# Kernel tuning notes

Hardware: AMD Instinct MI355X
Metric: run time of the kernel (lower is better)

## Reference

```python
import jax, jax.numpy as jnp
import numpy as np

IN_CH, OUT_CH, K = 4096, 4096, 64
C, F = IN_CH // K, OUT_CH // K  # 64, 64
BS = 256


def setup_inputs() -> dict:
    key = jax.random.key(0)
    k1, k2 = jax.random.split(key)
    x = jax.random.normal(k1, (BS, IN_CH), dtype=jnp.float32)
    stdv = 1.0 / float(np.sqrt(C))  # matches torch init: uniform(-1/sqrt(in_channels), ...)
    weights = jax.random.uniform(k2, (F, C, K), dtype=jnp.float32, minval=-stdv, maxval=stdv)
    return {"x": x, "weights": weights}


def reference(x, weights):
    # Faithful, batched version of Linear_BC_func.forward:
    #   per sample: ifft(fft(w, 'ortho') * fft(x, 'backward'), 'ortho').real, summed over C.
    # The per-sample Python loop and the C-sum are fused: sum over C is done in the
    # frequency domain (linearity of ifft), and the batch is handled by one einsum.
    bs = x.shape[0]
    f, c, k = weights.shape
    xk = x.reshape(bs, c, k)
    Wf = jnp.fft.fft(weights, norm="ortho")      # (F, C, K) complex64
    Xf = jnp.fft.fft(xk, norm="backward")        # (BS, C, K) complex64
    Sf = jnp.einsum("fck,bck->bfk", Wf, Xf)      # sum over C in frequency domain
    out = jnp.fft.ifft(Sf, norm="ortho").real.astype(jnp.float32)  # torch .float() keeps real part
    return out.reshape(bs, f * k)
```

## Files before the change

### kernel.cpp

```cpp
#include <hip/hip_runtime.h>


#define KDIM 4096

typedef __attribute__((ext_vector_type(8)))  short s16x8;
typedef __attribute__((ext_vector_type(4)))  float f32x4;
typedef __attribute__((ext_vector_type(16))) float f32x16;
typedef unsigned short u16;

__device__ __forceinline__ u16 f2bf(float f) {
  unsigned int u = __float_as_uint(f);
  u += 0x7FFF + ((u >> 16) & 1);
  return (u16)(u >> 16);
}

__global__ __launch_bounds__(256) void pack_kernel(const float* __restrict__ x,
                                                   u16* __restrict__ Xp) {
  __shared__ __align__(16) u16 tile[32 * 264];
  const int tid = threadIdx.x;
  const int rg  = blockIdx.x >> 4;
  const int cg  = blockIdx.x & 15;

  #pragma unroll
  for (int i = 0; i < 4; ++i) {
    int g    = i * 2048 + tid * 8;
    int row  = g >> 8;
    int kloc = g & 255;
    const float4* src = (const float4*)(x + (size_t)(rg * 32 + row) * 4096 + cg * 256 + kloc);
    float4 v0 = src[0], v1 = src[1];
    union { u16 u[8]; uint4 v; } o;
    o.u[0] = f2bf(v0.x); o.u[1] = f2bf(v0.y); o.u[2] = f2bf(v0.z); o.u[3] = f2bf(v0.w);
    o.u[4] = f2bf(v1.x); o.u[5] = f2bf(v1.y); o.u[6] = f2bf(v1.z); o.u[7] = f2bf(v1.w);
    *(uint4*)(tile + row * 264 + kloc) = o.v;
  }
  __syncthreads();

  const int lane = tid & 63;
  const int fw   = tid >> 6;
  #pragma unroll
  for (int i = 0; i < 4; ++i) {
    int fidx = i * 4 + fw;
    int cl   = fidx >> 2;
    int kk   = fidx & 3;
    int c    = cg * 4 + cl;
    uint4 v = *(const uint4*)(tile + (lane & 31) * 264 + cl * 64 + kk * 16 + (lane >> 5) * 8);
    size_t u = ((size_t)((c * 8 + rg) * 4 + kk) << 6) + lane;
    *(uint4*)(Xp + (u << 3)) = v;
  }
}

__global__ __launch_bounds__(1024, 4) void gemm_cnt(const u16* __restrict__ Xp,
                                                    const float* __restrict__ w,
                                                    float* __restrict__ out) {
  extern __shared__ __align__(16) char pool[];
  u16*   tab = (u16*)pool;
  float* red = (float*)pool;

  const int tid   = threadIdx.x;
  const int lane  = tid & 63;
  const int wid   = tid >> 6;
  const int cslot = wid & 7;
  const int half  = wid >> 3;
  const int l31   = lane & 31;
  const int lh    = lane >> 5;
  const int f     = blockIdx.x >> 2;
  const int q     = blockIdx.x & 3;
  const int rg    = q * 2 + half;

  const float* wf = w + ((size_t)f << 12);
  #pragma unroll
  for (int j = 0; j < 4; ++j) {
    int c = wid * 4 + j;
    u16 bv = f2bf(wf[(c << 6) + lane]);
    u16* T = tab + c * 576;
    #pragma unroll
    for (int m = 0; m < 8; ++m) {
      int i = (-(lane + m)) & 63;
      T[m * 72 + i] = bv;
    }
  }

  int bofs0, bofs1, bofs2, bofs3;
  {
    int i0;
    i0 = (lh * 8 - l31)      & 63; bofs0 = (i0 & 7) * 71 + i0;
    i0 = (lh * 8 - l31 - 16) & 63; bofs1 = (i0 & 7) * 71 + i0;
    i0 = (lh * 8 - l31 - 32) & 63; bofs2 = (i0 & 7) * 71 + i0;
    i0 = (lh * 8 - l31 - 48) & 63; bofs3 = (i0 & 7) * 71 + i0;
  }

  const u16* abase = Xp + ((size_t)(cslot * 8 + rg) * 2048 + lane * 8);

  s16x8 A0_0, A0_1, A0_2, A0_3;
  s16x8 A1_0, A1_1, A1_2, A1_3;
  s16x8 A2_0, A2_1, A2_2, A2_3;

  #define ALOAD(SET, T)                                                   \
    { const u16* nb_ = abase + (size_t)(T) * 131072;                      \
      asm volatile("global_load_dwordx4 %0, %4, off\n\t"                  \
                   "global_load_dwordx4 %1, %4, off offset:1024\n\t"      \
                   "global_load_dwordx4 %2, %4, off offset:2048\n\t"      \
                   "global_load_dwordx4 %3, %4, off offset:3072"          \
                   : "=&v"(A##SET##_0), "=&v"(A##SET##_1),                \
                     "=&v"(A##SET##_2), "=&v"(A##SET##_3)                 \
                   : "v"(nb_)); }

  #define WAITV_(N) asm volatile("s_waitcnt vmcnt(" #N ")")
  #define WAITV(N)  WAITV_(N)

  f32x16 acc0 = {}, acc1 = {};

  __syncthreads();

  ALOAD(0, 0)
  ALOAD(1, 1)

  #define STEP(T, CUR, PRE, DOPRE, WN)                                        \
    {                                                                         \
      if (DOPRE) ALOAD(PRE, (T) + 2)                                          \
      const u16* Tb = tab + (8 * (T) + cslot) * 576;                          \
      s16x8 b0 = *(const s16x8*)(Tb + bofs0);                                 \
      s16x8 b1 = *(const s16x8*)(Tb + bofs1);                                 \
      s16x8 b2 = *(const s16x8*)(Tb + bofs2);                                 \
      s16x8 b3 = *(const s16x8*)(Tb + bofs3);                                 \
      WAITV(WN);                                                              \
      __builtin_amdgcn_sched_barrier(0);                                      \
      acc0 = __builtin_amdgcn_mfma_f32_32x32x16_bf16(A##CUR##_0, b0, acc0, 0, 0, 0); \
      acc1 = __builtin_amdgcn_mfma_f32_32x32x16_bf16(A##CUR##_0, b2, acc1, 0, 0, 0); \
      acc0 = __builtin_amdgcn_mfma_f32_32x32x16_bf16(A##CUR##_1, b3, acc0, 0, 0, 0); \
      acc1 = __builtin_amdgcn_mfma_f32_32x32x16_bf16(A##CUR##_1, b1, acc1, 0, 0, 0); \
      acc0 = __builtin_amdgcn_mfma_f32_32x32x16_bf16(A##CUR##_2, b2, acc0, 0, 0, 0); \
      acc1 = __builtin_amdgcn_mfma_f32_32x32x16_bf16(A##CUR##_2, b0, acc1, 0, 0, 0); \
      acc0 = __builtin_amdgcn_mfma_f32_32x32x16_bf16(A##CUR##_3, b1, acc0, 0, 0, 0); \
      acc1 = __builtin_amdgcn_mfma_f32_32x32x16_bf16(A##CUR##_3, b3, acc1, 0, 0, 0); \
    }

  STEP(0, 0, 2, 1, 8)
  STEP(1, 1, 0, 1, 8)
  STEP(2, 2, 1, 1, 8)
  STEP(3, 0, 2, 1, 8)
  STEP(4, 1, 0, 1, 8)
  STEP(5, 2, 1, 1, 8)
  STEP(6, 0, 2, 0, 4)
  STEP(7, 1, 2, 0, 0)

  __syncthreads();
  {
    float* slot = red + wid * 2048;
    #pragma unroll
    for (int i = 0; i < 4; ++i) {
      f32x4 v0 = {acc0[4*i], acc0[4*i+1], acc0[4*i+2], acc0[4*i+3]};
      f32x4 v1 = {acc1[4*i], acc1[4*i+1], acc1[4*i+2], acc1[4*i+3]};
      *(f32x4*)(slot + ((i)     * 64 + lane) * 4) = v0;
      *(f32x4*)(slot + ((i + 4) * 64 + lane) * 4) = v1;
    }
  }
  __syncthreads();
  {
    const int rhalf = tid >> 9;
    const int ii    = (tid >> 6) & 7;
    const int sl    = tid & 63;
    f32x4 s = {};
    #pragma unroll
    for (int cs = 0; cs < 8; ++cs)
      s += *(const f32x4*)(red + (size_t)(rhalf * 8 + cs) * 2048 + (ii * 64 + sl) * 4);
    const int col  = (f << 6) + (ii >> 2) * 32 + (sl & 31);
    const int rowb = q * 64 + rhalf * 32 + 4 * (sl >> 5) + 8 * (ii & 3);
    #pragma unroll
    for (int e = 0; e < 4; ++e)
      out[(size_t)(rowb + e) * 4096 + col] = s[e];
  }
}

extern "C" void kernel_launch(void* const* d_in, const int* in_sizes, int n_in,
                              void* d_out, int out_size, void* d_ws, size_t ws_size,
                              hipStream_t stream) {
  const float* x = (const float*)d_in[0];
  const float* w = (const float*)d_in[1];
  float* out = (float*)d_out;

  u16* Xp = (u16*)d_ws;

  pack_kernel<<<128, 256, 0, stream>>>(x, Xp);
  gemm_cnt<<<256, 1024, 131072, stream>>>(Xp, w, out);
}
```

Baseline: 19.24 us.

## Retile circulant GEMM so each block covers two filters and 32 batch rows

```diff
diff --git a/kernel.cpp b/kernel.cpp
--- a/kernel.cpp
+++ b/kernel.cpp
@@ -49,9 +49,9 @@
   }
 }
 
-__global__ __launch_bounds__(1024, 4) void gemm_cnt(const u16* __restrict__ Xp,
-                                                    const float* __restrict__ w,
-                                                    float* __restrict__ out) {
+__global__ __launch_bounds__(1024, 4) void gemm_f2(const u16* __restrict__ Xp,
+                                                   const float* __restrict__ w,
+                                                   float* __restrict__ out) {
   extern __shared__ __align__(16) char pool[];
   u16*   tab = (u16*)pool;
   float* red = (float*)pool;
@@ -59,20 +59,20 @@
   const int tid   = threadIdx.x;
   const int lane  = tid & 63;
   const int wid   = tid >> 6;
-  const int cslot = wid & 7;
-  const int half  = wid >> 3;
+  const int cg    = wid & 1;
+  const int kg    = wid >> 1;
   const int l31   = lane & 31;
   const int lh    = lane >> 5;
-  const int f     = blockIdx.x >> 2;
-  const int q     = blockIdx.x & 3;
-  const int rg    = q * 2 + half;
+  const int q     = blockIdx.x & 7;
+  const int fg    = blockIdx.x >> 3;
 
-  const float* wf = w + ((size_t)f << 12);
   #pragma unroll
-  for (int j = 0; j < 4; ++j) {
-    int c = wid * 4 + j;
-    u16 bv = f2bf(wf[(c << 6) + lane]);
-    u16* T = tab + c * 576;
+  for (int j = 0; j < 8; ++j) {
+    int t    = wid * 8 + j;
+    int fidx = t >> 6;
+    int c    = t & 63;
+    u16 bv = f2bf(w[((size_t)(fg * 2 + fidx) << 12) + (c << 6) + lane]);
+    u16* T = tab + t * 576;
     #pragma unroll
     for (int m = 0; m < 8; ++m) {
       int i = (-(lane + m)) & 63;
@@ -89,14 +89,15 @@
     i0 = (lh * 8 - l31 - 48) & 63; bofs3 = (i0 & 7) * 71 + i0;
   }
 
-  const u16* abase = Xp + ((size_t)(cslot * 8 + rg) * 2048 + lane * 8);
+  const u16* abase = Xp + ((size_t)kg * 8 * 16384 + q * 2048 + lane * 8);
+  const u16* tabf  = tab + cg * 36864;
 
   s16x8 A0_0, A0_1, A0_2, A0_3;
   s16x8 A1_0, A1_1, A1_2, A1_3;
   s16x8 A2_0, A2_1, A2_2, A2_3;
 
   #define ALOAD(SET, T)                                                   \
-    { const u16* nb_ = abase + (size_t)(T) * 131072;                      \
+    { const u16* nb_ = abase + (size_t)(T) * 16384;                       \
       asm volatile("global_load_dwordx4 %0, %4, off\n\t"                  \
                    "global_load_dwordx4 %1, %4, off offset:1024\n\t"      \
                    "global_load_dwordx4 %2, %4, off offset:2048\n\t"      \
@@ -118,7 +119,7 @@
   #define STEP(T, CUR, PRE, DOPRE, WN)                                        \
     {                                                                         \
       if (DOPRE) ALOAD(PRE, (T) + 2)                                          \
-      const u16* Tb = tab + (8 * (T) + cslot) * 576;                          \
+      const u16* Tb = tabf + (kg * 8 + (T)) * 576;                            \
       s16x8 b0 = *(const s16x8*)(Tb + bofs0);                                 \
       s16x8 b1 = *(const s16x8*)(Tb + bofs1);                                 \
       s16x8 b2 = *(const s16x8*)(Tb + bofs2);                                 \
@@ -146,7 +147,7 @@
 
   __syncthreads();
   {
-    float* slot = red + wid * 2048;
+    float* slot = red + (cg * 8 + kg) * 2048;
     #pragma unroll
     for (int i = 0; i < 4; ++i) {
       f32x4 v0 = {acc0[4*i], acc0[4*i+1], acc0[4*i+2], acc0[4*i+3]};
@@ -157,15 +158,15 @@
   }
   __syncthreads();
   {
-    const int rhalf = tid >> 9;
-    const int ii    = (tid >> 6) & 7;
-    const int sl    = tid & 63;
+    const int rcg = tid >> 9;
+    const int ii  = (tid >> 6) & 7;
+    const int sl  = tid & 63;
     f32x4 s = {};
     #pragma unroll
-    for (int cs = 0; cs < 8; ++cs)
-      s += *(const f32x4*)(red + (size_t)(rhalf * 8 + cs) * 2048 + (ii * 64 + sl) * 4);
-    const int col  = (f << 6) + (ii >> 2) * 32 + (sl & 31);
-    const int rowb = q * 64 + rhalf * 32 + 4 * (sl >> 5) + 8 * (ii & 3);
+    for (int k = 0; k < 8; ++k)
+      s += *(const f32x4*)(red + (size_t)(rcg * 8 + k) * 2048 + (ii * 64 + sl) * 4);
+    const int col  = ((fg * 2 + rcg) << 6) + (ii >> 2) * 32 + (sl & 31);
+    const int rowb = q * 32 + 8 * (ii & 3) + 4 * (sl >> 5);
     #pragma unroll
     for (int e = 0; e < 4; ++e)
       out[(size_t)(rowb + e) * 4096 + col] = s[e];
@@ -182,5 +183,5 @@
   u16* Xp = (u16*)d_ws;
 
   pack_kernel<<<128, 256, 0, stream>>>(x, Xp);
-  gemm_cnt<<<256, 1024, 131072, stream>>>(Xp, w, out);
+  gemm_f2<<<256, 1024, 147456, stream>>>(Xp, w, out);
 }
```

New measurement: 19.74 us, median of 4. 2.6% more time.
